# Kernel tuning notes

Measured on AMD Instinct MI355X. Metric: run time of the kernel, lower is better.

The kernel has to match this reference:

```python
import jax, jax.numpy as jnp
import numpy as np

H = 768
NH = 12
HD = H // NH
NDIM = 5
LN_EPS = 1e-5


def setup_inputs() -> dict:
    key = jax.random.key(0)
    ks = jax.random.split(key, 12)
    B, S = 4, 2048
    xavier = lambda k: jax.random.uniform(k, (H, H), jnp.float32, -1.0, 1.0) * np.sqrt(6.0 / (H + H))
    return {
        "hidden_states": jax.random.normal(ks[0], (B, S, H), jnp.float32),
        "Wq": xavier(ks[1]), "bq": jnp.zeros((H,), jnp.float32),
        "Wk": xavier(ks[2]), "bk": jnp.zeros((H,), jnp.float32),
        "Wv": xavier(ks[3]), "bv": jnp.zeros((H,), jnp.float32),
        "Wo": xavier(ks[4]), "bo": jnp.zeros((H,), jnp.float32),
        # per-dimension, per-head scalar biases (torch init: zeros; use small randn so grads are non-trivial)
        "dim_biases": 0.02 * jax.random.normal(ks[5], (NDIM, NH), jnp.float32),
        "ln_gamma": jnp.ones((H,), jnp.float32),
        "ln_beta": jnp.zeros((H,), jnp.float32),
        "attention_mask": jax.random.randint(ks[6], (4, 2048), 0, 2, jnp.int32),
        "dimension_idx": 2,
    }


def reference(hidden_states, Wq, bq, Wk, bk, Wv, bv, Wo, bo, dim_biases,
              ln_gamma, ln_beta, attention_mask, dimension_idx):
    B, S, _ = hidden_states.shape
    residual = hidden_states
    # torch nn.Linear: x @ W.T + b
    q = (hidden_states @ Wq.T + bq).reshape(B, S, NH, HD).transpose(0, 2, 1, 3)  # [B,NH,S,HD]
    k = (hidden_states @ Wk.T + bk).reshape(B, S, NH, HD).transpose(0, 2, 1, 3)
    v = (hidden_states @ Wv.T + bv).reshape(B, S, NH, HD).transpose(0, 2, 1, 3)

    scores = jnp.einsum("bhqd,bhkd->bhqk", q, k) / np.sqrt(HD)  # [B,NH,S,S]
    if dimension_idx is not None and dimension_idx < NDIM:
        scores = scores + dim_biases[dimension_idx][None, :, None, None]
    # mask over key positions, broadcast over heads and queries
    scores = jnp.where(attention_mask[:, None, None, :] == 0, -jnp.inf, scores)
    attn = jax.nn.softmax(scores, axis=-1)

    ctx = jnp.einsum("bhqk,bhkd->bhqd", attn, v)  # [B,NH,S,HD]
    ctx = ctx.transpose(0, 2, 1, 3).reshape(B, S, H)
    out = ctx @ Wo.T + bo

    y = out + residual
    mu = jnp.mean(y, axis=-1, keepdims=True)
    var = jnp.var(y, axis=-1, keepdims=True)
    y = (y - mu) / jnp.sqrt(var + LN_EPS) * ln_gamma + ln_beta
    return y
```

## Files before the change

### kernel.cpp

```cpp
#include <hip/hip_runtime.h>
#include <hip/hip_bf16.h>

#define HH    768
#define NHEAD 12
#define HDIM  64
#define BB    4
#define SS    2048
#define MM    (BB*SS)
#define NDIMS 5
#define WEL   (HH*HH)
#define LOG2E 1.44269504088896f
#define QSCALE 0.180336881f

typedef unsigned short u16;
typedef __attribute__((ext_vector_type(8))) short short8;
typedef __attribute__((ext_vector_type(4))) short short4v;
typedef __attribute__((ext_vector_type(4))) float floatx4;
typedef __attribute__((ext_vector_type(16))) float floatx16;
typedef __attribute__((ext_vector_type(4))) unsigned int uint4v;
typedef __attribute__((ext_vector_type(2))) unsigned int uint2v;

__device__ __forceinline__ float bf2f(u16 u) {
    return __uint_as_float(((unsigned int)u) << 16);
}
__device__ __forceinline__ u16 f2bf(float f) {
    unsigned int x = __float_as_uint(f);
    unsigned int r = (x + 0x7fffu + ((x >> 16) & 1u)) >> 16;
    return (u16)r;
}
__device__ __forceinline__ unsigned int pack_bf16x2(float a, float b) {
    float2 f2 = make_float2(a, b);
    __hip_bfloat162 h2 = __float22bfloat162_rn(f2);
    return *reinterpret_cast<unsigned int*>(&h2);
}
__device__ __forceinline__ void gld16(const u16* g, u16* l) {
    __builtin_amdgcn_global_load_lds(
        (const __attribute__((address_space(1))) unsigned int*)g,
        (__attribute__((address_space(3))) unsigned int*)l, 16, 0, 0);
}

__global__ __launch_bounds__(256) void f32_to_bf16(
    const float* __restrict__ in, u16* __restrict__ out, int n8)
{
    int i = blockIdx.x * 256 + threadIdx.x;
    if (i >= n8) return;
    float4 a = ((const float4*)in)[i*2];
    float4 b = ((const float4*)in)[i*2 + 1];
    ushort4 lo, hi;
    lo.x = f2bf(a.x); lo.y = f2bf(a.y); lo.z = f2bf(a.z); lo.w = f2bf(a.w);
    hi.x = f2bf(b.x); hi.y = f2bf(b.y); hi.z = f2bf(b.z); hi.w = f2bf(b.w);
    ((ushort4*)out)[i*2]     = lo;
    ((ushort4*)out)[i*2 + 1] = hi;
}

#define XCVT_BLKS ((MM*HH)/8/256)
#define WCVT_BLKS (WEL/8/256)
__global__ __launch_bounds__(256) void cvt_all(
    const float* __restrict__ x,
    const float* __restrict__ W0, const float* __restrict__ W1,
    const float* __restrict__ W2, const float* __restrict__ W3,
    u16* __restrict__ xb, u16* __restrict__ wb)
{
    const int bid = blockIdx.x;
    const float* src;
    u16* dst;
    int i;
    if (bid < XCVT_BLKS) {
        src = x; dst = xb; i = bid * 256 + threadIdx.x;
    } else {
        const int wsel = (bid - XCVT_BLKS) / WCVT_BLKS;
        src = (wsel == 0) ? W0 : (wsel == 1) ? W1 : (wsel == 2) ? W2 : W3;
        dst = wb + (size_t)wsel * WEL;
        i = ((bid - XCVT_BLKS) % WCVT_BLKS) * 256 + threadIdx.x;
    }
    float4 a = ((const float4*)src)[i*2];
    float4 b = ((const float4*)src)[i*2 + 1];
    ushort4 lo, hi;
    lo.x = f2bf(a.x); lo.y = f2bf(a.y); lo.z = f2bf(a.z); lo.w = f2bf(a.w);
    hi.x = f2bf(b.x); hi.y = f2bf(b.y); hi.z = f2bf(b.z); hi.w = f2bf(b.w);
    ((ushort4*)dst)[i*2]     = lo;
    ((ushort4*)dst)[i*2 + 1] = hi;
}

__global__ __launch_bounds__(256, 3) void gemm_gld_qkv(
    const u16* __restrict__ Xb, const u16* __restrict__ Wb3,
    const float* __restrict__ bq, const float* __restrict__ bk, const float* __restrict__ bv,
    u16* __restrict__ oq, u16* __restrict__ ok, u16* __restrict__ ov)
{
    __shared__ u16 Xs[128][64];
    __shared__ u16 Ws[192][64];
    const int t = threadIdx.x;
    const int w = t >> 6, lane = t & 63;
    const int wy = w >> 1, wx = w & 1;
    const int m = lane & 31, hh = lane >> 5;
    const int grow = lane >> 3;
    const int cg   = (lane & 7) ^ grow;

    const int flat = blockIdx.x + 12 * blockIdx.y;
    const int swz  = (flat & 7) * 96 + (flat >> 3);
    const int j0 = (swz % 12) * 192;
    const int i0 = (swz / 12) * 128;
    const int sel = j0 / HH;
    const int lj  = j0 - sel * HH;
    const float* biasL = ((sel == 0) ? bq : (sel == 1) ? bk : bv) + lj;
    u16* outL = ((sel == 0) ? oq : (sel == 1) ? ok : ov) + lj;
    const u16* Wrows = Wb3 + (size_t)j0 * HH;

    floatx16 acc[2][3];
    #pragma unroll
    for (int am = 0; am < 2; ++am)
        #pragma unroll
        for (int bn = 0; bn < 3; ++bn)
            #pragma unroll
            for (int r = 0; r < 16; ++r) acc[am][bn][r] = 0.f;

    for (int k0 = 0; k0 < HH; k0 += 64) {
        __syncthreads();
        #pragma unroll
        for (int j = 0; j < 4; ++j) {
            const int r = w*32 + j*8;
            gld16(Xb + (size_t)(i0 + r + grow)*HH + k0 + cg*8, &Xs[r][0]);
        }
        #pragma unroll
        for (int j = 0; j < 6; ++j) {
            const int r = w*48 + j*8;
            gld16(Wrows + (size_t)(r + grow)*HH + k0 + cg*8, &Ws[r][0]);
        }
        __syncthreads();

        #pragma unroll
        for (int kh = 0; kh < 4; ++kh) {
            const int ch = kh*2 + hh;
            short8 af[2], bf[3];
            #pragma unroll
            for (int am = 0; am < 2; ++am) {
                const int row = wy*64 + am*32 + m;
                af[am] = *(const short8*)&Xs[row][(ch ^ (m & 7))*8];
            }
            #pragma unroll
            for (int bn = 0; bn < 3; ++bn) {
                const int row = wx*96 + bn*32 + m;
                bf[bn] = *(const short8*)&Ws[row][(ch ^ (m & 7))*8];
            }
            #pragma unroll
            for (int am = 0; am < 2; ++am)
                #pragma unroll
                for (int bn = 0; bn < 3; ++bn)
                    acc[am][bn] = __builtin_amdgcn_mfma_f32_32x32x16_bf16(
                        af[am], bf[bn], acc[am][bn], 0, 0, 0);
        }
    }

    float bb[3];
    #pragma unroll
    for (int bn = 0; bn < 3; ++bn) bb[bn] = biasL[wx*96 + bn*32 + m];
    #pragma unroll
    for (int am = 0; am < 2; ++am)
        #pragma unroll
        for (int bn = 0; bn < 3; ++bn)
            #pragma unroll
            for (int r = 0; r < 16; ++r) {
                int row = i0 + wy*64 + am*32 + (r & 3) + 8*(r >> 2) + 4*hh;
                outL[(size_t)row*HH + wx*96 + bn*32 + m] = f2bf(acc[am][bn][r] + bb[bn]);
            }
}

__global__ __launch_bounds__(256) void gemm_gld_m64(
    const u16* __restrict__ Xb, const u16* __restrict__ Wb,
    const float* __restrict__ bias, u16* __restrict__ out)
{
    __shared__ u16 Xs[64][64];
    __shared__ u16 Ws[128][64];
    const int t = threadIdx.x;
    const int w = t >> 6, lane = t & 63;
    const int m = lane & 31, hh = lane >> 5;
    const int grow = lane >> 3;
    const int cg   = (lane & 7) ^ grow;

    const int flat = blockIdx.x + 6 * blockIdx.y;
    const int swz  = (flat & 7) * 96 + (flat >> 3);
    const int j0 = (swz % 6) * 128;
    const int i0 = (swz / 6) * 64;

    floatx16 acc[2];
    #pragma unroll
    for (int am = 0; am < 2; ++am)
        #pragma unroll
        for (int r = 0; r < 16; ++r) acc[am][r] = 0.f;

    for (int k0 = 0; k0 < HH; k0 += 64) {
        __syncthreads();
        #pragma unroll
        for (int j = 0; j < 2; ++j) {
            const int r = w*16 + j*8;
            gld16(Xb + (size_t)(i0 + r + grow)*HH + k0 + cg*8, &Xs[r][0]);
        }
        #pragma unroll
        for (int j = 0; j < 4; ++j) {
            const int r = w*32 + j*8;
            gld16(Wb + (size_t)(j0 + r + grow)*HH + k0 + cg*8, &Ws[r][0]);
        }
        __syncthreads();

        #pragma unroll
        for (int kh = 0; kh < 4; ++kh) {
            const int ch = kh*2 + hh;
            short8 af[2], bf;
            af[0] = *(const short8*)&Xs[m][(ch ^ (m & 7))*8];
            af[1] = *(const short8*)&Xs[32 + m][(ch ^ (m & 7))*8];
            bf    = *(const short8*)&Ws[w*32 + m][(ch ^ (m & 7))*8];
            acc[0] = __builtin_amdgcn_mfma_f32_32x32x16_bf16(af[0], bf, acc[0], 0, 0, 0);
            acc[1] = __builtin_amdgcn_mfma_f32_32x32x16_bf16(af[1], bf, acc[1], 0, 0, 0);
        }
    }

    const float bb = bias[j0 + w*32 + m];
    #pragma unroll
    for (int am = 0; am < 2; ++am)
        #pragma unroll
        for (int r = 0; r < 16; ++r) {
            int row = i0 + am*32 + (r & 3) + 8*(r >> 2) + 4*hh;
            out[(size_t)row*HH + j0 + w*32 + m] = f2bf(acc[am][r] + bb);
        }
}

__global__ __launch_bounds__(256) void gemm_mfma_nt(
    const u16* __restrict__ Xb, const float* __restrict__ W,
    const float* __restrict__ bias, u16* __restrict__ out)
{
    __shared__ u16 Xs[128][40];
    __shared__ u16 Wt[64][40];
    const int t = threadIdx.x;
    const int w = t >> 6, lane = t & 63;
    const int c = lane & 15, qd = lane >> 4;
    const int i0 = blockIdx.y * 128, j0 = blockIdx.x * 64;
    const int xrow = t >> 1, xoff = (t & 1) * 16;
    const int wn = t >> 2, woff = (t & 3) * 8;

    floatx4 acc[2][4];
    #pragma unroll
    for (int mt = 0; mt < 2; ++mt)
        #pragma unroll
        for (int nt = 0; nt < 4; ++nt) acc[mt][nt] = (floatx4){0.f,0.f,0.f,0.f};

    for (int k0 = 0; k0 < HH; k0 += 32) {
        uint4 xa  = *(const uint4*)(Xb + (size_t)(i0 + xrow)*HH + k0 + xoff);
        uint4 xb2 = *(const uint4*)(Xb + (size_t)(i0 + xrow)*HH + k0 + xoff + 8);
        float4 wa = *(const float4*)(W + (size_t)(j0 + wn)*HH + k0 + woff);
        float4 wb = *(const float4*)(W + (size_t)(j0 + wn)*HH + k0 + woff + 4);
        __syncthreads();
        *(uint4*)&Xs[xrow][xoff]     = xa;
        *(uint4*)&Xs[xrow][xoff + 8] = xb2;
        ushort4 w0, w1;
        w0.x = f2bf(wa.x); w0.y = f2bf(wa.y); w0.z = f2bf(wa.z); w0.w = f2bf(wa.w);
        w1.x = f2bf(wb.x); w1.y = f2bf(wb.y); w1.z = f2bf(wb.z); w1.w = f2bf(wb.w);
        *(ushort4*)&Wt[wn][woff]     = w0;
        *(ushort4*)&Wt[wn][woff + 4] = w1;
        __syncthreads();

        short8 a0 = *(const short8*)&Xs[w*32 + c][qd*8];
        short8 a1 = *(const short8*)&Xs[w*32 + 16 + c][qd*8];
        #pragma unroll
        for (int nt = 0; nt < 4; ++nt) {
            short8 bfr = *(const short8*)&Wt[nt*16 + c][qd*8];
            acc[0][nt] = __builtin_amdgcn_mfma_f32_16x16x32_bf16(a0, bfr, acc[0][nt], 0, 0, 0);
            acc[1][nt] = __builtin_amdgcn_mfma_f32_16x16x32_bf16(a1, bfr, acc[1][nt], 0, 0, 0);
        }
    }

    float bv[4];
    #pragma unroll
    for (int nt = 0; nt < 4; ++nt) bv[nt] = bias[j0 + nt*16 + c];
    #pragma unroll
    for (int mt = 0; mt < 2; ++mt)
        #pragma unroll
        for (int nt = 0; nt < 4; ++nt)
            #pragma unroll
            for (int r = 0; r < 4; ++r)
                out[(size_t)(i0 + w*32 + mt*16 + qd*4 + r)*HH + j0 + nt*16 + c] =
                    f2bf(acc[mt][nt][r] + bv[nt]);
}

__global__ __launch_bounds__(256, 3) void attn_mfma32(
    const u16* __restrict__ Q, const u16* __restrict__ K, const u16* __restrict__ V,
    const float* __restrict__ dim_biases, const int* __restrict__ mask,
    const int* __restrict__ dim_idx_p, u16* __restrict__ ctx)
{
    __shared__ u16 Ks[2][64][64];
    __shared__ u16 Vt[2][64][68];
    __shared__ float madd[2][64];

    const int t = threadIdx.x;
    const int w = t >> 6, lane = t & 63;
    const int ql = lane & 31, hi = lane >> 5;
    const int sw7 = ql & 7;

    const int flat = blockIdx.x + 16 * (blockIdx.y + 12 * blockIdx.z);
    const int swz  = (flat & 7) * 96 + (flat >> 3);
    const int q0 = (swz & 15) * 128;
    const int h  = (swz >> 4) % NHEAD;
    const int b  = swz / (16 * NHEAD);

    const int didx = *dim_idx_p;
    const float db2 = ((didx < NDIMS) ? dim_biases[didx*NHEAD + h] : 0.f) * LOG2E;

    const int grow = lane >> 3;
    const int cg   = (lane & 7) ^ grow;
    const int vkp = t & 31;
    const int vdg = (t >> 5) * 8;

    short8 ones;
    #pragma unroll
    for (int j = 0; j < 8; ++j) ones[j] = (short)0x3F80;

    short8 qv[4];
    {
        const u16* qsrc = Q + ((size_t)(b*SS + q0 + w*32 + ql))*HH + h*HDIM + 8*hi;
        #pragma unroll
        for (int s = 0; s < 4; ++s) {
            ushort4 u0 = *(const ushort4*)(qsrc + s*16);
            ushort4 u1 = *(const ushort4*)(qsrc + s*16 + 4);
            const u16 uu[8] = {u0.x,u0.y,u0.z,u0.w,u1.x,u1.y,u1.z,u1.w};
            #pragma unroll
            for (int j = 0; j < 8; ++j)
                qv[s][j] = (short)f2bf(bf2f(uu[j]) * QSCALE);
        }
    }

    floatx16 o[2], lacc;
    #pragma unroll
    for (int r = 0; r < 16; ++r) { o[0][r] = 0.f; o[1][r] = 0.f; lacc[r] = 0.f; }

    uint4 VA, VB;
    int mreg = 0;

    auto issueK = [&](int kt, int buf) {
        #pragma unroll
        for (int j = 0; j < 2; ++j) {
            const int rbase = w*16 + j*8;
            gld16(K + (size_t)(b*SS + kt*64 + rbase + grow)*HH + h*HDIM + cg*8,
                  &Ks[buf][rbase][0]);
        }
    };
    auto issueV = [&](int kt) {
        const u16* va = V + ((size_t)(b*SS + kt*64 + 2*vkp))*HH + h*HDIM + vdg;
        VA = *(const uint4*)va;
        VB = *(const uint4*)(va + HH);
        if (t < 64) mreg = mask[(size_t)b*SS + kt*64 + t];
    };
    auto writeV = [&](int buf) {
        const unsigned* Aw = (const unsigned*)&VA;
        const unsigned* Bw = (const unsigned*)&VB;
        #pragma unroll
        for (int i2 = 0; i2 < 4; ++i2) {
            unsigned a = Aw[i2], bb = Bw[i2];
            *(unsigned*)&Vt[buf][vdg + 2*i2][2*vkp]     = (a & 0xffffu) | (bb << 16);
            *(unsigned*)&Vt[buf][vdg + 2*i2 + 1][2*vkp] = (a >> 16) | (bb & 0xffff0000u);
        }
        if (t < 64) madd[buf][t] = (mreg != 0) ? db2 : -1e30f;
    };

    issueK(0, 0);
    issueV(0);
    writeV(0);

    for (int kt = 0; kt < SS/64; ++kt) {
        const int cur = kt & 1;
        __syncthreads();
        const bool more = (kt + 1 < SS/64);
        if (more) { issueK(kt + 1, cur ^ 1); issueV(kt + 1); }

        #pragma unroll
        for (int kblk = 0; kblk < 2; ++kblk) {
            const u16* kb = &Ks[cur][kblk*32 + ql][0];

            floatx16 z;
            #pragma unroll
            for (int qq = 0; qq < 4; ++qq) {
                float4 mv = *(const float4*)&madd[cur][kblk*32 + qq*8 + 4*hi];
                z[qq*4+0] = mv.x; z[qq*4+1] = mv.y; z[qq*4+2] = mv.z; z[qq*4+3] = mv.w;
            }
            short8 kf[4];
            #pragma unroll
            for (int s = 0; s < 4; ++s)
                kf[s] = *(const short8*)(kb + ((s*2 + hi) ^ sw7)*8);
            __builtin_amdgcn_s_setprio(1);
            #pragma unroll
            for (int s = 0; s < 4; ++s)
                z = __builtin_amdgcn_mfma_f32_32x32x16_bf16(kf[s], qv[s], z, 0, 0, 0);
            __builtin_amdgcn_s_setprio(0);

            #pragma unroll
            for (int r = 0; r < 16; ++r) z[r] = __builtin_amdgcn_exp2f(z[r]);

            #pragma unroll
            for (int ks = 0; ks < 2; ++ks) {
                unsigned x0 = pack_bf16x2(z[ks*8 + 0], z[ks*8 + 1]);
                unsigned y0 = pack_bf16x2(z[ks*8 + 4], z[ks*8 + 5]);
                unsigned x1 = pack_bf16x2(z[ks*8 + 2], z[ks*8 + 3]);
                unsigned y1 = pack_bf16x2(z[ks*8 + 6], z[ks*8 + 7]);
                uint2v s0 = __builtin_amdgcn_permlane32_swap(x0, y0, false, false);
                uint2v s1 = __builtin_amdgcn_permlane32_swap(x1, y1, false, false);
                uint4v pv; pv[0] = s0[0]; pv[1] = s1[0]; pv[2] = s0[1]; pv[3] = s1[1];
                short8 pa = __builtin_bit_cast(short8, pv);

                const int ck = kblk*4 + ks*2 + hi;
                const u16* vp0 = &Vt[cur][ql][ck*8];
                const u16* vp1 = &Vt[cur][32 + ql][ck*8];
                short4v a0 = *(const short4v*)vp0;
                short4v a1 = *(const short4v*)(vp0 + 4);
                short4v b0 = *(const short4v*)vp1;
                short4v b1 = *(const short4v*)(vp1 + 4);
                short8 vf0, vf1;
                #pragma unroll
                for (int j = 0; j < 4; ++j) {
                    vf0[j] = a0[j]; vf0[4+j] = a1[j];
                    vf1[j] = b0[j]; vf1[4+j] = b1[j];
                }

                __builtin_amdgcn_s_setprio(1);
                lacc = __builtin_amdgcn_mfma_f32_32x32x16_bf16(pa, ones, lacc, 0, 0, 0);
                o[0] = __builtin_amdgcn_mfma_f32_32x32x16_bf16(pa, vf0, o[0], 0, 0, 0);
                o[1] = __builtin_amdgcn_mfma_f32_32x32x16_bf16(pa, vf1, o[1], 0, 0, 0);
                __builtin_amdgcn_s_setprio(0);
            }
        }

        if (more) writeV(cur ^ 1);
    }

    #pragma unroll
    for (int r = 0; r < 16; ++r) {
        float l = lacc[r];
        float inv = (l > 0.f) ? 1.f / l : 0.f;
        const int qrow = q0 + w*32 + (r & 3) + 8*(r >> 2) + 4*hi;
        u16* dst = ctx + ((size_t)(b*SS + qrow))*HH + h*HDIM + ql;
        dst[0]  = f2bf(o[0][r] * inv);
        dst[32] = f2bf(o[1][r] * inv);
    }
}

__global__ __launch_bounds__(256) void add_ln_wave(
    const u16* __restrict__ proj, const float* __restrict__ resid,
    const float* __restrict__ gamma, const float* __restrict__ beta,
    float* __restrict__ out)
{
    const int t = threadIdx.x, w = t >> 6, lane = t & 63;
    const int row = blockIdx.x * 4 + w;
    const size_t base = (size_t)row * HH + lane * 12;
    const int gbase = lane * 12;

    float x[12];
    #pragma unroll
    for (int j = 0; j < 3; ++j) {
        ushort4 p = *(const ushort4*)(proj + base + j*4);
        float4  r = *(const float4*)(resid + base + j*4);
        x[j*4+0] = bf2f(p.x) + r.x;
        x[j*4+1] = bf2f(p.y) + r.y;
        x[j*4+2] = bf2f(p.z) + r.z;
        x[j*4+3] = bf2f(p.w) + r.w;
    }
    float s = 0.f, ss = 0.f;
    #pragma unroll
    for (int j = 0; j < 12; ++j) { s += x[j]; ss += x[j]*x[j]; }
    #pragma unroll
    for (int off = 1; off < 64; off <<= 1) {
        s  += __shfl_xor(s, off);
        ss += __shfl_xor(ss, off);
    }
    float mean = s * (1.f/768.f);
    float var  = ss * (1.f/768.f) - mean*mean;
    float rstd = rsqrtf(fmaxf(var, 0.f) + 1e-5f);
    #pragma unroll
    for (int j = 0; j < 3; ++j) {
        float4 g = *(const float4*)(gamma + gbase + j*4);
        float4 bt = *(const float4*)(beta + gbase + j*4);
        float4 y;
        y.x = (x[j*4+0]-mean)*rstd*g.x + bt.x;
        y.y = (x[j*4+1]-mean)*rstd*g.y + bt.y;
        y.z = (x[j*4+2]-mean)*rstd*g.z + bt.z;
        y.w = (x[j*4+3]-mean)*rstd*g.w + bt.w;
        *(float4*)(out + base + j*4) = y;
    }
}

extern "C" void kernel_launch(void* const* d_in, const int* in_sizes, int n_in,
                              void* d_out, int out_size, void* d_ws, size_t ws_size,
                              hipStream_t stream)
{
    (void)in_sizes; (void)n_in; (void)out_size;
    const float* x    = (const float*)d_in[0];
    const float* Wq   = (const float*)d_in[1];
    const float* bq   = (const float*)d_in[2];
    const float* Wk   = (const float*)d_in[3];
    const float* bk   = (const float*)d_in[4];
    const float* Wv   = (const float*)d_in[5];
    const float* bv   = (const float*)d_in[6];
    const float* Wo   = (const float*)d_in[7];
    const float* bo   = (const float*)d_in[8];
    const float* dimb = (const float*)d_in[9];
    const float* gam  = (const float*)d_in[10];
    const float* bet  = (const float*)d_in[11];
    const int* mask   = (const int*)d_in[12];
    const int* didx   = (const int*)d_in[13];

    const size_t N = (size_t)MM * HH;
    if (ws_size < 4 * N * sizeof(u16)) return;
    u16* ws = (u16*)d_ws;
    u16* q    = ws;
    u16* kbuf = ws + N;
    u16* vbuf = ws + 2*N;
    u16* slot3 = ws + 3*N;
    u16* xb   = slot3;
    u16* ctx  = slot3;
    u16* proj = q;

    const bool bigws = ws_size >= (4 * N + 4 * (size_t)WEL) * sizeof(u16);
    u16* wb = ws + 4 * N;

    if (bigws) {
        cvt_all<<<XCVT_BLKS + 4*WCVT_BLKS, 256, 0, stream>>>(x, Wq, Wk, Wv, Wo, xb, wb);
        gemm_gld_qkv<<<dim3(3*HH/192, MM/128), 256, 0, stream>>>(
            xb, wb, bq, bk, bv, q, kbuf, vbuf);
    } else {
        f32_to_bf16<<<(int)(N/8/256), 256, 0, stream>>>(x, xb, (int)(N/8));
        dim3 gg(HH/64, MM/128);
        gemm_mfma_nt<<<gg, 256, 0, stream>>>(xb, Wq, bq, q);
        gemm_mfma_nt<<<gg, 256, 0, stream>>>(xb, Wk, bk, kbuf);
        gemm_mfma_nt<<<gg, 256, 0, stream>>>(xb, Wv, bv, vbuf);
    }
    attn_mfma32<<<dim3(SS/128, NHEAD, BB), 256, 0, stream>>>(q, kbuf, vbuf, dimb, mask, didx, ctx);
    if (bigws) gemm_gld_m64<<<dim3(HH/128, MM/64), 256, 0, stream>>>(ctx, wb + 3*WEL, bo, proj);
    else {
        dim3 gg(HH/64, MM/128);
        gemm_mfma_nt<<<gg, 256, 0, stream>>>(ctx, Wo, bo, proj);
    }
    add_ln_wave<<<MM/4, 256, 0, stream>>>(proj, x, gam, bet, (float*)d_out);
}
```

Measured before the change: 237.3 us.

## Pre-transpose V into a head-major layout and load it asynchronously in attention

Adds a separate kernel that transposes V into a [B,NH,HD,S] layout, so the attention kernel can fetch V tiles with the same direct global-to-LDS path used for K. This replaces the per-iteration register staging, in-kernel transpose and padded LDS stores, and the short4 V-fragment loads become swizzled 16-byte LDS reads. The cost is an extra kernel launch and a full read/write pass over V. Workspace slots are reassigned so the ctx output reuses the V buffer.

```diff
diff --git a/kernel.cpp b/kernel.cpp
--- a/kernel.cpp
+++ b/kernel.cpp
@@ -14,7 +14,6 @@
 
 typedef unsigned short u16;
 typedef __attribute__((ext_vector_type(8))) short short8;
-typedef __attribute__((ext_vector_type(4))) short short4v;
 typedef __attribute__((ext_vector_type(4))) float floatx4;
 typedef __attribute__((ext_vector_type(16))) float floatx16;
 typedef __attribute__((ext_vector_type(4))) unsigned int uint4v;
@@ -82,6 +81,35 @@
     ((ushort4*)dst)[i*2 + 1] = hi;
 }
 
+__global__ __launch_bounds__(256) void v_transpose(
+    const u16* __restrict__ V, u16* __restrict__ vt)
+{
+    __shared__ unsigned Ls[64][36];
+    const int t = threadIdx.x;
+    const int kt = blockIdx.x, h = blockIdx.y, b = blockIdx.z;
+    const int p  = t & 31;
+    const int dg = (t >> 5) * 8;
+    const u16* va = V + ((size_t)(b*SS + kt*64 + 2*p))*HH + h*HDIM + dg;
+    const u16* vb = va + HH;
+    uint4 A = *(const uint4*)va;
+    uint4 Bv = *(const uint4*)vb;
+    const unsigned* Aw = (const unsigned*)&A;
+    const unsigned* Bw = (const unsigned*)&Bv;
+    #pragma unroll
+    for (int i = 0; i < 4; ++i) {
+        unsigned a = Aw[i], c = Bw[i];
+        Ls[dg + 2*i][p]     = (a & 0xffffu) | (c << 16);
+        Ls[dg + 2*i + 1][p] = (a >> 16) | (c & 0xffff0000u);
+    }
+    __syncthreads();
+    const int d = t >> 2, kc = (t & 3) * 8;
+    uint4 o0 = *(const uint4*)&Ls[d][kc];
+    uint4 o1 = *(const uint4*)&Ls[d][kc + 4];
+    u16* dst = vt + ((size_t)((b*NHEAD + h)*HDIM + d))*SS + kt*64 + kc*2;
+    *(uint4*)dst       = o0;
+    *(uint4*)(dst + 8) = o1;
+}
+
 __global__ __launch_bounds__(256, 3) void gemm_gld_qkv(
     const u16* __restrict__ Xb, const u16* __restrict__ Wb3,
     const float* __restrict__ bq, const float* __restrict__ bk, const float* __restrict__ bv,
@@ -282,12 +310,12 @@
 }
 
 __global__ __launch_bounds__(256, 3) void attn_mfma32(
-    const u16* __restrict__ Q, const u16* __restrict__ K, const u16* __restrict__ V,
+    const u16* __restrict__ Q, const u16* __restrict__ K, const u16* __restrict__ vt,
     const float* __restrict__ dim_biases, const int* __restrict__ mask,
     const int* __restrict__ dim_idx_p, u16* __restrict__ ctx)
 {
     __shared__ u16 Ks[2][64][64];
-    __shared__ u16 Vt[2][64][68];
+    __shared__ u16 Vs[2][64][64];
     __shared__ float madd[2][64];
 
     const int t = threadIdx.x;
@@ -306,8 +334,8 @@
 
     const int grow = lane >> 3;
     const int cg   = (lane & 7) ^ grow;
-    const int vkp = t & 31;
-    const int vdg = (t >> 5) * 8;
+
+    const u16* Vrows = vt + (size_t)(b*NHEAD + h)*HDIM*SS;
 
     short8 ones;
     #pragma unroll
@@ -331,44 +359,34 @@
     #pragma unroll
     for (int r = 0; r < 16; ++r) { o[0][r] = 0.f; o[1][r] = 0.f; lacc[r] = 0.f; }
 
-    uint4 VA, VB;
     int mreg = 0;
 
-    auto issueK = [&](int kt, int buf) {
+    auto issueKV = [&](int kt, int buf) {
         #pragma unroll
         for (int j = 0; j < 2; ++j) {
             const int rbase = w*16 + j*8;
             gld16(K + (size_t)(b*SS + kt*64 + rbase + grow)*HH + h*HDIM + cg*8,
                   &Ks[buf][rbase][0]);
+            gld16(Vrows + (size_t)(rbase + grow)*SS + kt*64 + cg*8,
+                  &Vs[buf][rbase][0]);
         }
     };
-    auto issueV = [&](int kt) {
-        const u16* va = V + ((size_t)(b*SS + kt*64 + 2*vkp))*HH + h*HDIM + vdg;
-        VA = *(const uint4*)va;
-        VB = *(const uint4*)(va + HH);
+    auto issueM = [&](int kt) {
         if (t < 64) mreg = mask[(size_t)b*SS + kt*64 + t];
     };
-    auto writeV = [&](int buf) {
-        const unsigned* Aw = (const unsigned*)&VA;
-        const unsigned* Bw = (const unsigned*)&VB;
-        #pragma unroll
-        for (int i2 = 0; i2 < 4; ++i2) {
-            unsigned a = Aw[i2], bb = Bw[i2];
-            *(unsigned*)&Vt[buf][vdg + 2*i2][2*vkp]     = (a & 0xffffu) | (bb << 16);
-            *(unsigned*)&Vt[buf][vdg + 2*i2 + 1][2*vkp] = (a >> 16) | (bb & 0xffff0000u);
-        }
+    auto writeM = [&](int buf) {
         if (t < 64) madd[buf][t] = (mreg != 0) ? db2 : -1e30f;
     };
 
-    issueK(0, 0);
-    issueV(0);
-    writeV(0);
+    issueKV(0, 0);
+    issueM(0);
+    writeM(0);
 
     for (int kt = 0; kt < SS/64; ++kt) {
         const int cur = kt & 1;
         __syncthreads();
         const bool more = (kt + 1 < SS/64);
-        if (more) { issueK(kt + 1, cur ^ 1); issueV(kt + 1); }
+        if (more) { issueKV(kt + 1, cur ^ 1); issueM(kt + 1); }
 
         #pragma unroll
         for (int kblk = 0; kblk < 2; ++kblk) {
@@ -405,18 +423,8 @@
                 short8 pa = __builtin_bit_cast(short8, pv);
 
                 const int ck = kblk*4 + ks*2 + hi;
-                const u16* vp0 = &Vt[cur][ql][ck*8];
-                const u16* vp1 = &Vt[cur][32 + ql][ck*8];
-                short4v a0 = *(const short4v*)vp0;
-                short4v a1 = *(const short4v*)(vp0 + 4);
-                short4v b0 = *(const short4v*)vp1;
-                short4v b1 = *(const short4v*)(vp1 + 4);
-                short8 vf0, vf1;
-                #pragma unroll
-                for (int j = 0; j < 4; ++j) {
-                    vf0[j] = a0[j]; vf0[4+j] = a1[j];
-                    vf1[j] = b0[j]; vf1[4+j] = b1[j];
-                }
+                short8 vf0 = *(const short8*)&Vs[cur][ql][(ck ^ sw7)*8];
+                short8 vf1 = *(const short8*)&Vs[cur][32 + ql][(ck ^ sw7)*8];
 
                 __builtin_amdgcn_s_setprio(1);
                 lacc = __builtin_amdgcn_mfma_f32_32x32x16_bf16(pa, ones, lacc, 0, 0, 0);
@@ -426,7 +434,7 @@
             }
         }
 
-        if (more) writeV(cur ^ 1);
+        if (more) writeM(cur ^ 1);
     }
 
     #pragma unroll
@@ -512,7 +520,8 @@
     u16* vbuf = ws + 2*N;
     u16* slot3 = ws + 3*N;
     u16* xb   = slot3;
-    u16* ctx  = slot3;
+    u16* vtb  = slot3;
+    u16* ctx  = vbuf;
     u16* proj = q;
 
     const bool bigws = ws_size >= (4 * N + 4 * (size_t)WEL) * sizeof(u16);
@@ -529,7 +538,8 @@
         gemm_mfma_nt<<<gg, 256, 0, stream>>>(xb, Wk, bk, kbuf);
         gemm_mfma_nt<<<gg, 256, 0, stream>>>(xb, Wv, bv, vbuf);
     }
-    attn_mfma32<<<dim3(SS/128, NHEAD, BB), 256, 0, stream>>>(q, kbuf, vbuf, dimb, mask, didx, ctx);
+    v_transpose<<<dim3(SS/64, NHEAD, BB), 256, 0, stream>>>(vbuf, vtb);
+    attn_mfma32<<<dim3(SS/128, NHEAD, BB), 256, 0, stream>>>(q, kbuf, vtb, dimb, mask, didx, ctx);
     if (bigws) gemm_gld_m64<<<dim3(HH/128, MM/64), 256, 0, stream>>>(ctx, wb + 3*WEL, bo, proj);
     else {
         dim3 gg(HH/64, MM/128);
```

Measured after the change: 242.5 us. 2.2% more time.
